# Kernel tuning notes

Hardware: AMD Instinct MI355X
Metric: run time of the kernel (lower is better)

## Reference

```python
import jax, jax.numpy as jnp
import numpy as np

ALPHA = 0.2  # LeakyReLU negative slope
NEG_INF = -1e12


def setup_inputs() -> dict:
    key = jax.random.key(0)
    k1, k2, k3, k4 = jax.random.split(key, 4)
    B, N, F_in, F_out = 8, 4096, 128, 64
    inp = jax.random.normal(k1, (B, N, F_in), dtype=jnp.float32)
    adj = jax.random.randint(k2, (B, N, N), 0, 2, dtype=jnp.int32)
    # xavier-uniform-ish init for W, a
    W = jax.random.normal(k3, (F_in, F_out), dtype=jnp.float32) * (2.0 / (F_in + F_out)) ** 0.5
    a = jax.random.normal(k4, (2 * F_out, 1), dtype=jnp.float32) * (2.0 / (2 * F_out + 1)) ** 0.5
    return {"inp": inp, "adj": adj, "W": W, "a": a}


def reference(inp, adj, W, a):
    # inp: [B,N,F_in], adj: [B,N,N] int, W: [F_in,F_out], a: [2*F_out,1]
    F_out = W.shape[1]
    h = jnp.einsum('bnf,fo->bno', inp, W)          # [B,N,F_out]
    a1 = a[:F_out, 0]                              # [F_out]
    a2 = a[F_out:, 0]                              # [F_out]
    # e[b,i,j] = leakyrelu(h_i . a1 + h_j . a2)  (== concat([h_i,h_j]) @ a)
    s1 = h @ a1                                    # [B,N]
    s2 = h @ a2                                    # [B,N]
    e = s1[:, :, None] + s2[:, None, :]            # [B,N,N]
    e = jnp.where(e > 0, e, ALPHA * e)             # LeakyReLU
    att = jnp.where(adj > 0, e, NEG_INF)
    att = jax.nn.softmax(att, axis=-1)             # [B,N,N]
    # dropout p=0.0 -> identity
    h_prime = jnp.einsum('bij,bjo->bio', att, h)   # [B,N,F_out]
    return jax.nn.elu(h_prime)
```

## Files before the change

kernel.cpp:

```cpp
#include <hip/hip_runtime.h>
#include <hip/hip_bf16.h>
#include <cstdint>

typedef __attribute__((ext_vector_type(8))) short short8;
typedef __attribute__((ext_vector_type(4))) float floatx4;

#define LEAKY_ALPHA 0.2f

__device__ __forceinline__ unsigned short f2bf_rne(float f) {
    unsigned u = __float_as_uint(f);
    unsigned r = u + 0x7FFFu + ((u >> 16) & 1u);
    return (unsigned short)(r >> 16);
}

__global__ __launch_bounds__(256) void k_h(const float* __restrict__ inp,
                                           const float* __restrict__ W,
                                           const float* __restrict__ a,
                                           unsigned short* __restrict__ hT,
                                           float* __restrict__ s1,
                                           float* __restrict__ s2) {
    __shared__ float hs[64][65];
    const int tid  = threadIdx.x;
    const int wv   = tid >> 6;
    const int lane = tid & 63;
    const int blk  = blockIdx.x;
    const int b     = blk >> 6;
    const int ibase = (blk & 63) * 64;

    const float a1 = a[lane];
    const float a2 = a[64 + lane];

    for (int rr = 0; rr < 16; ++rr) {
        const int rloc = wv * 16 + rr;
        const int row  = ibase + rloc;
        const float* ip = inp + ((size_t)(b * 4096 + row)) * 128;
        float acc = 0.f;
        #pragma unroll
        for (int f = 0; f < 128; f += 4) {
            float4 v = *(const float4*)(ip + f);
            acc += v.x * W[(f + 0) * 64 + lane];
            acc += v.y * W[(f + 1) * 64 + lane];
            acc += v.z * W[(f + 2) * 64 + lane];
            acc += v.w * W[(f + 3) * 64 + lane];
        }
        hs[rloc][lane] = acc;
        float r1 = acc * a1;
        float r2 = acc * a2;
        #pragma unroll
        for (int off = 32; off > 0; off >>= 1) {
            r1 += __shfl_xor(r1, off);
            r2 += __shfl_xor(r2, off);
        }
        if (lane == 0) {
            s1[b * 4096 + row] = r1;
            s2[b * 4096 + row] = r2;
        }
    }
    __syncthreads();

    const int o    = tid & 63;
    const int half = tid >> 6;
    const int tl   = half >> 1;
    const int nco  = (half & 1) * 16;
    unsigned pk[8];
    #pragma unroll
    for (int s = 0; s < 16; s += 2) {
        unsigned lo = f2bf_rne(hs[tl * 32 + nco + s    ][o]);
        unsigned hi = f2bf_rne(hs[tl * 32 + nco + s + 1][o]);
        pk[s >> 1] = lo | (hi << 16);
    }
    const int tile = (ibase >> 5) + tl;
    unsigned short* dst = hT + (((size_t)b * 128 + tile) * 64 + o) * 32 + nco;
    *(int4*)(dst)     = *(int4*)&pk[0];
    *(int4*)(dst + 8) = *(int4*)&pk[4];
}

__global__ __launch_bounds__(256, 4) void k_fused(const int* __restrict__ adj,
                                                  const unsigned short* __restrict__ hT,
                                                  const float* __restrict__ s1g,
                                                  const float* __restrict__ s2g,
                                                  float* __restrict__ out) {
    __shared__ unsigned maskw[32][129];
    __shared__ float s2s[4096];

    const int tid   = threadIdx.x;
    const int b     = blockIdx.x >> 7;
    const int rtile = blockIdx.x & 127;
    const int wv    = tid >> 6;
    const int lane  = tid & 63;

    {
        const float* src = s2g + b * 4096;
        #pragma unroll
        for (int t = 0; t < 4; ++t) {
            int idx = tid * 16 + t * 4;
            *(float4*)&s2s[idx] = *(const float4*)(src + idx);
        }
    }

    {
        const int* abase = adj + ((size_t)(b * 4096 + rtile * 32)) * 4096
                         + (size_t)wv * 32768;
        #pragma unroll 2
        for (int i = 0; i < 16; ++i) {
            const int* p = abase + i * 2048 + lane * 32;
            unsigned w = 0;
            #pragma unroll
            for (int k = 0; k < 8; ++k) {
                const int4 v = *(const int4*)(p + k * 4);
                w |= (v.x > 0 ? 1u : 0u) << (k * 4 + 0);
                w |= (v.y > 0 ? 1u : 0u) << (k * 4 + 1);
                w |= (v.z > 0 ? 1u : 0u) << (k * 4 + 2);
                w |= (v.w > 0 ? 1u : 0u) << (k * 4 + 3);
            }
            maskw[wv * 8 + (i >> 1)][(i & 1) * 64 + lane] = w;
        }
    }
    __syncthreads();

    const int jhalf = wv >> 1;
    const int m     = lane & 15;
    const int kh    = lane >> 4;
    const int rl    = (wv & 1) * 16 + m;
    const int rbase = rtile * 32 + (wv & 1) * 16;
    const int row   = rbase + m;

    const float s1v = s1g[b * 4096 + row];
    const int jb0 = jhalf * 2048 + kh * 8;
    const unsigned* mrow = &maskw[rl][jhalf * 64];

    const unsigned short* hbase =
        hT + (((size_t)b * 128 + jhalf * 64) * 64 + m) * 32 + kh * 8;
    const unsigned short* hrow0 = hbase;
    const unsigned short* hrow1 = hbase + 512;
    const unsigned short* hrow2 = hbase + 1024;
    const unsigned short* hrow3 = hbase + 1536;

    floatx4 acc0 = (floatx4){0.f,0.f,0.f,0.f};
    floatx4 acc1 = (floatx4){0.f,0.f,0.f,0.f};
    floatx4 acc2 = (floatx4){0.f,0.f,0.f,0.f};
    floatx4 acc3 = (floatx4){0.f,0.f,0.f,0.f};
    float lsum = 0.f;

    unsigned rm_0, rm_1;
    short8 rb0_0, rb1_0, rb2_0, rb3_0, rb0_1, rb1_1, rb2_1, rb3_1;

    rm_0  = mrow[0];
    rb0_0 = *(const short8*)(hrow0);         rb1_0 = *(const short8*)(hrow1);
    rb2_0 = *(const short8*)(hrow2);         rb3_0 = *(const short8*)(hrow3);
    rm_1  = mrow[1];
    rb0_1 = *(const short8*)(hrow0 + 2048);  rb1_1 = *(const short8*)(hrow1 + 2048);
    rb2_1 = *(const short8*)(hrow2 + 2048);  rb3_1 = *(const short8*)(hrow3 + 2048);

#define GAT_STEP(SL, STEPIDX)                                                  \
    do {                                                                       \
        const unsigned cmw = rm_##SL;                                          \
        const short8 cb0 = rb0_##SL, cb1 = rb1_##SL;                           \
        const short8 cb2 = rb2_##SL, cb3 = rb3_##SL;                           \
        const int pstep = ((STEPIDX) + 2) & 63;         \
        const int poff = pstep * 2048;                         \
        rm_##SL  = mrow[pstep];                                                \
        rb0_##SL = *(const short8*)(hrow0 + poff);                             \
        rb1_##SL = *(const short8*)(hrow1 + poff);                             \
        rb2_##SL = *(const short8*)(hrow2 + poff);                             \
        rb3_##SL = *(const short8*)(hrow3 + poff);                             \
        const int soff = jb0 + (STEPIDX) * 32;                                 \
        const float4 csa = *(const float4*)&s2s[soff];                         \
        const float4 csb = *(const float4*)&s2s[soff + 4];                     \
        const unsigned mb = (cmw >> (kh * 8)) & 0xffu;                         \
        const float sv[8] = {csa.x, csa.y, csa.z, csa.w,                       \
                             csb.x, csb.y, csb.z, csb.w};                      \
        short8 af;                                                             \
        float psum = 0.f;                                                      \
        _Pragma("unroll")                                                      \
        for (int t = 0; t < 8; ++t) {                                          \
            float e = s1v + sv[t];                                             \
            e = fmaxf(e, LEAKY_ALPHA * e);                                     \
            float pv = ((mb >> t) & 1u) ? __expf(e) : 0.f;                     \
            psum += pv;                                                        \
            af[t] = (short)f2bf_rne(pv);                                       \
        }                                                                      \
        lsum += psum;                                                          \
        acc0 = __builtin_amdgcn_mfma_f32_16x16x32_bf16(af, cb0, acc0, 0,0,0);  \
        acc1 = __builtin_amdgcn_mfma_f32_16x16x32_bf16(af, cb1, acc1, 0,0,0);  \
        acc2 = __builtin_amdgcn_mfma_f32_16x16x32_bf16(af, cb2, acc2, 0,0,0);  \
        acc3 = __builtin_amdgcn_mfma_f32_16x16x32_bf16(af, cb3, acc3, 0,0,0);  \
    } while (0)

    #pragma unroll 1
    for (int it = 0; it < 32; ++it) {
        const int s0 = it * 2;
        GAT_STEP(0, s0);
        GAT_STEP(1, s0 + 1);
    }
#undef GAT_STEP

    lsum += __shfl_xor(lsum, 16);
    lsum += __shfl_xor(lsum, 32);

    floatx4 accs[4] = {acc0, acc1, acc2, acc3};

    float* accb = (float*)&maskw[0][0];
    float* lb   = accb + 2 * 64 * 17;

    __syncthreads();
    if (wv >= 2) {
        #pragma unroll
        for (int f = 0; f < 4; ++f)
            #pragma unroll
            for (int r = 0; r < 4; ++r)
                accb[(wv - 2) * 64 * 17 + lane * 17 + f * 4 + r] = accs[f][r];
        lb[(wv - 2) * 64 + lane] = lsum;
    }
    __syncthreads();
    if (wv < 2) {
        const float ltot = lsum + lb[wv * 64 + lane];
        #pragma unroll
        for (int f = 0; f < 4; ++f) {
            #pragma unroll
            for (int r = 0; r < 4; ++r) {
                float v = accs[f][r] + accb[wv * 64 * 17 + lane * 17 + f * 4 + r];
                const int drow = (lane >> 4) * 4 + r;
                const float lr = __shfl(ltot, drow);
                const float hp = v / lr;
                const float o  = (hp > 0.f) ? hp : (__expf(hp) - 1.f);
                out[((size_t)(b * 4096 + rbase + drow)) * 64 + f * 16 + (lane & 15)] = o;
            }
        }
    }
}

extern "C" void kernel_launch(void* const* d_in, const int* in_sizes, int n_in,
                              void* d_out, int out_size, void* d_ws, size_t ws_size,
                              hipStream_t stream) {
    const float* inp = (const float*)d_in[0];
    const int*   adj = (const int*)d_in[1];
    const float* W   = (const float*)d_in[2];
    const float* a   = (const float*)d_in[3];
    float* out = (float*)d_out;

    unsigned short* hT = (unsigned short*)d_ws;
    float* s1 = (float*)((char*)d_ws + (size_t)8 * 64 * 4096 * 2);
    float* s2 = s1 + 8 * 4096;

    k_h<<<512, 256, 0, stream>>>(inp, W, a, hT, s1, s2);
    k_fused<<<1024, 256, 0, stream>>>(adj, hT, s1, s2, out);
}
```

Measured before the change: 812.0 us.

## Factor attention exponent into precomputed per-node exponentials, removing per-edge exp

Uses exp(leaky(s1+s2)) = exp(s1)·exp(s2) when the sum is positive and exp(αs1)·exp(αs2) otherwise. k_h now precomputes these per-node exponentials: fp32 for rows and packed fp16 for columns. The inner attention loop then does two multiplies and a select instead of an exp per edge. It also switches to the packed bf16 conversion intrinsic. This trades transcendental work in the hot loop for fp16 rounding of the column factors and a possible overflow risk for large scores.

After: 815.6 us. Within noise of the previous version (+0.4%).

```diff
diff --git a/kernel.cpp b/kernel.cpp
--- a/kernel.cpp
+++ b/kernel.cpp
@@ -1,5 +1,6 @@
 #include <hip/hip_runtime.h>
 #include <hip/hip_bf16.h>
+#include <hip/hip_fp16.h>
 #include <cstdint>
 
 typedef __attribute__((ext_vector_type(8))) short short8;
@@ -13,12 +14,23 @@
     return (unsigned short)(r >> 16);
 }
 
+__device__ __forceinline__ unsigned pk2bf(float lo, float hi) {
+    union { __hip_bfloat162 b; unsigned u; } c;
+    c.b = __float22bfloat162_rn(make_float2(lo, hi));
+    return c.u;
+}
+
+__device__ __forceinline__ float2 h2f2(unsigned w) {
+    union { unsigned u; __half2 h; } c; c.u = w;
+    return __half22float2(c.h);
+}
+
 __global__ __launch_bounds__(256) void k_h(const float* __restrict__ inp,
                                            const float* __restrict__ W,
                                            const float* __restrict__ a,
                                            unsigned short* __restrict__ hT,
-                                           float* __restrict__ s1,
-                                           float* __restrict__ s2) {
+                                           float2* __restrict__ e1,
+                                           __half2* __restrict__ e2h) {
     __shared__ float hs[64][65];
     const int tid  = threadIdx.x;
     const int wv   = tid >> 6;
@@ -52,8 +64,8 @@
             r2 += __shfl_xor(r2, off);
         }
         if (lane == 0) {
-            s1[b * 4096 + row] = r1;
-            s2[b * 4096 + row] = r2;
+            e1[b * 4096 + row]  = make_float2(__expf(r1), __expf(LEAKY_ALPHA * r1));
+            e2h[b * 4096 + row] = __floats2half2_rn(__expf(r2), __expf(LEAKY_ALPHA * r2));
         }
     }
     __syncthreads();
@@ -77,11 +89,11 @@
 
 __global__ __launch_bounds__(256, 4) void k_fused(const int* __restrict__ adj,
                                                   const unsigned short* __restrict__ hT,
-                                                  const float* __restrict__ s1g,
-                                                  const float* __restrict__ s2g,
+                                                  const float2* __restrict__ e1g,
+                                                  const __half2* __restrict__ e2hg,
                                                   float* __restrict__ out) {
     __shared__ unsigned maskw[32][129];
-    __shared__ float s2s[4096];
+    __shared__ __half2 e2s[4096];
 
     const int tid   = threadIdx.x;
     const int b     = blockIdx.x >> 7;
@@ -90,11 +102,11 @@
     const int lane  = tid & 63;
 
     {
-        const float* src = s2g + b * 4096;
+        const __half2* src = e2hg + b * 4096;
         #pragma unroll
         for (int t = 0; t < 4; ++t) {
             int idx = tid * 16 + t * 4;
-            *(float4*)&s2s[idx] = *(const float4*)(src + idx);
+            *(int4*)&e2s[idx] = *(const int4*)(src + idx);
         }
     }
 
@@ -125,7 +137,8 @@
     const int rbase = rtile * 32 + (wv & 1) * 16;
     const int row   = rbase + m;
 
-    const float s1v = s1g[b * 4096 + row];
+    const float2 E1 = e1g[b * 4096 + row];
+    const float E1p = E1.x, E1n = E1.y;
     const int jb0 = jhalf * 2048 + kh * 8;
     const unsigned* mrow = &maskw[rl][jhalf * 64];
 
@@ -151,6 +164,17 @@
     rm_1  = mrow[1];
     rb0_1 = *(const short8*)(hrow0 + 2048);  rb1_1 = *(const short8*)(hrow1 + 2048);
     rb2_1 = *(const short8*)(hrow2 + 2048);  rb3_1 = *(const short8*)(hrow3 + 2048);
+
+#define GAT_COL(WRD, T)                                                        \
+    {                                                                          \
+        const float2 ef = h2f2((unsigned)(WRD));                               \
+        const float P  = E1p * ef.x;                                           \
+        const float Nn = E1n * ef.y;                                           \
+        float p = (P > 1.0f) ? P : Nn;                                         \
+        p = ((mb >> (T)) & 1u) ? p : 0.0f;                                     \
+        psum += p;                                                             \
+        pv[T] = p;                                                             \
+    }
 
 #define GAT_STEP(SL, STEPIDX)                                                  \
     do {                                                                       \
@@ -165,22 +189,19 @@
         rb2_##SL = *(const short8*)(hrow2 + poff);                             \
         rb3_##SL = *(const short8*)(hrow3 + poff);                             \
         const int soff = jb0 + (STEPIDX) * 32;                                 \
-        const float4 csa = *(const float4*)&s2s[soff];                         \
-        const float4 csb = *(const float4*)&s2s[soff + 4];                     \
+        const int4 eA = *(const int4*)&e2s[soff];                              \
+        const int4 eB = *(const int4*)&e2s[soff + 4];                          \
         const unsigned mb = (cmw >> (kh * 8)) & 0xffu;                         \
-        const float sv[8] = {csa.x, csa.y, csa.z, csa.w,                       \
-                             csb.x, csb.y, csb.z, csb.w};                      \
-        short8 af;                                                             \
+        float pv[8];                                                           \
         float psum = 0.f;                                                      \
-        _Pragma("unroll")                                                      \
-        for (int t = 0; t < 8; ++t) {                                          \
-            float e = s1v + sv[t];                                             \
-            e = fmaxf(e, LEAKY_ALPHA * e);                                     \
-            float pv = ((mb >> t) & 1u) ? __expf(e) : 0.f;                     \
-            psum += pv;                                                        \
-            af[t] = (short)f2bf_rne(pv);                                       \
-        }                                                                      \
+        GAT_COL(eA.x, 0) GAT_COL(eA.y, 1) GAT_COL(eA.z, 2) GAT_COL(eA.w, 3)    \
+        GAT_COL(eB.x, 4) GAT_COL(eB.y, 5) GAT_COL(eB.z, 6) GAT_COL(eB.w, 7)    \
         lsum += psum;                                                          \
+        int4 ai;                                                               \
+        ai.x = pk2bf(pv[0], pv[1]); ai.y = pk2bf(pv[2], pv[3]);                \
+        ai.z = pk2bf(pv[4], pv[5]); ai.w = pk2bf(pv[6], pv[7]);                \
+        union { int4 i; short8 s; } cc; cc.i = ai;                             \
+        const short8 af = cc.s;                                                \
         acc0 = __builtin_amdgcn_mfma_f32_16x16x32_bf16(af, cb0, acc0, 0,0,0);  \
         acc1 = __builtin_amdgcn_mfma_f32_16x16x32_bf16(af, cb1, acc1, 0,0,0);  \
         acc2 = __builtin_amdgcn_mfma_f32_16x16x32_bf16(af, cb2, acc2, 0,0,0);  \
@@ -194,6 +215,7 @@
         GAT_STEP(1, s0 + 1);
     }
 #undef GAT_STEP
+#undef GAT_COL
 
     lsum += __shfl_xor(lsum, 16);
     lsum += __shfl_xor(lsum, 32);
@@ -240,9 +262,9 @@
     float* out = (float*)d_out;
 
     unsigned short* hT = (unsigned short*)d_ws;
-    float* s1 = (float*)((char*)d_ws + (size_t)8 * 64 * 4096 * 2);
-    float* s2 = s1 + 8 * 4096;
-
-    k_h<<<512, 256, 0, stream>>>(inp, W, a, hT, s1, s2);
-    k_fused<<<1024, 256, 0, stream>>>(adj, hT, s1, s2, out);
-}
+    float2*  e1  = (float2*)((char*)d_ws + (size_t)4 * 1024 * 1024);
+    __half2* e2h = (__half2*)((char*)d_ws + (size_t)4 * 1024 * 1024 + 262144);
+
+    k_h<<<512, 256, 0, stream>>>(inp, W, a, hT, e1, e2h);
+    k_fused<<<1024, 256, 0, stream>>>(adj, hT, e1, e2h, out);
+}
```
